# Performance work log

Hardware: AMD Instinct MI355X
Metric: run time of the kernel (lower is better)

## Reference

```python
import jax, jax.numpy as jnp
import numpy as np

N_NODES = 50000
N_EDGES = 800000
IN_FEAT = 128
HEADS = 4
UNITS = 16
LEAKY_ALPHA = 0.2  # tf.nn.leaky_relu default


def setup_inputs() -> dict:
    key = jax.random.key(0)
    k1, k2, k3, k4, k5 = jax.random.split(key, 5)
    x = jax.random.normal(k1, (N_NODES, IN_FEAT), dtype=jnp.float32)
    edge_index = jax.random.randint(k2, (N_EDGES, 2), 0, N_NODES, dtype=jnp.int32)
    # Dense kernel (glorot-ish scaling), no bias (use_bias=False)
    W = jax.random.normal(k3, (IN_FEAT, HEADS * UNITS), dtype=jnp.float32) * (1.0 / np.sqrt(IN_FEAT))
    glorot = np.sqrt(2.0 / (1 + UNITS)).astype(np.float32)
    att_w1 = jax.random.normal(k4, (HEADS, 1, UNITS), dtype=jnp.float32) * glorot
    att_w2 = jax.random.normal(k5, (HEADS, 1, UNITS), dtype=jnp.float32) * glorot
    return {"x": x, "edge_index": edge_index, "W": W, "att_w1": att_w1, "att_w2": att_w2}


def reference(x, edge_index, W, att_w1, att_w2):
    n_nodes = x.shape[0]
    h = x @ W  # [N, H*U]
    snd_idx = edge_index[:, 0]
    rcv_idx = edge_index[:, 1]
    # gather per-edge features, split into heads -> [H, E, U]
    sender = h[snd_idx].reshape(-1, HEADS, UNITS).transpose(1, 0, 2)
    receiver = h[rcv_idx].reshape(-1, HEADS, UNITS).transpose(1, 0, 2)
    # per-edge, per-head attention logits [H, E]
    att = jnp.sum(att_w1 * sender, axis=-1) + jnp.sum(att_w2 * receiver, axis=-1)
    att = jnp.where(att > 0, att, LEAKY_ALPHA * att)
    # segment softmax over receiver neighborhoods, per head
    seg_max = jax.vmap(lambda a: jax.ops.segment_max(a, rcv_idx, num_segments=n_nodes))(att)  # [H, N]
    e = jnp.exp(att - seg_max[:, rcv_idx])
    denom = jax.vmap(lambda a: jax.ops.segment_sum(a, rcv_idx, num_segments=n_nodes))(e)  # [H, N]
    alpha = e / denom[:, rcv_idx]  # [H, E]
    # weighted scatter-sum of sender features -> [H, N, U]
    out = jax.vmap(lambda v: jax.ops.segment_sum(v, rcv_idx, num_segments=n_nodes))(sender * alpha[:, :, None])
    # concat heads -> [N, H*U]; activation is None (identity)
    return out.transpose(1, 0, 2).reshape(n_nodes, HEADS * UNITS)
```

## Files before the change

kernel.cpp:

```cpp
#include <hip/hip_runtime.h>
#include <math.h>

#define N_NODES 50000
#define N_EDGES 800000
#define IN_FEAT 128
#define HEADS   4
#define UNITS   16
#define OUTF    64
#define LEAKY   0.2f

#define CAP     64
#define GEMM_BLKS 782
#define A_BLOCKS  391
#define EPB     8

typedef __attribute__((ext_vector_type(8))) short bf16x8;
typedef __attribute__((ext_vector_type(4))) float f32x4;

__device__ __forceinline__ unsigned short f2bf(float f) {
    unsigned u = __float_as_uint(f);
    unsigned r = u + 0x7FFFu + ((u >> 16) & 1u);
    return (unsigned short)(r >> 16);
}

__global__ __launch_bounds__(256) void prep(const float* __restrict__ W,
                                            unsigned short* __restrict__ Wt_g,
                                            int* __restrict__ node_cnt) {
    int idx = blockIdx.x * 256 + threadIdx.x;
    if (idx < N_NODES) node_cnt[idx] = 0;
    if (idx < IN_FEAT * OUTF) {
        int k = idx >> 6, c = idx & 63;
        Wt_g[c * IN_FEAT + k] = f2bf(W[idx]);
    }
}

__global__ __launch_bounds__(256) void fused_gemm_scatter(const float* __restrict__ x,
                                                          const unsigned short* __restrict__ Wt_g,
                                                          const float* __restrict__ w1,
                                                          const float* __restrict__ w2,
                                                          const int2* __restrict__ ei,
                                                          unsigned short* __restrict__ hg,
                                                          float* __restrict__ a1,
                                                          float* __restrict__ a2,
                                                          int* __restrict__ node_cnt,
                                                          int* __restrict__ csr) {
    const int t = threadIdx.x;

    if (blockIdx.x >= GEMM_BLKS) {
        const int e0 = (blockIdx.x - GEMM_BLKS) * 2048;
        #pragma unroll
        for (int j = 0; j < EPB; ++j) {
            int e = e0 + t + j * 256;
            if (e < N_EDGES) {
                int2 ed = ei[e];
                int p = atomicAdd(&node_cnt[ed.y], 1);
                if (p < CAP) csr[(size_t)ed.y * CAP + p] = ed.x;
            }
        }
        return;
    }

    __shared__ unsigned short xl[64 * 136];
    __shared__ unsigned short wt[64 * 136];

    const int node0 = blockIdx.x * 64;

    #pragma unroll
    for (int it = 0; it < 8; ++it) {
        int idx = t + 256 * it;
        int r = idx >> 5, q = idx & 31;
        int node = node0 + r;
        float4 v = make_float4(0.f, 0.f, 0.f, 0.f);
        if (node < N_NODES) v = *(const float4*)(x + (size_t)node * IN_FEAT + q * 4);
        ushort4 b;
        b.x = f2bf(v.x); b.y = f2bf(v.y); b.z = f2bf(v.z); b.w = f2bf(v.w);
        *(ushort4*)&xl[r * 136 + q * 4] = b;
    }
    {
        const ushort4* Wt4 = (const ushort4*)Wt_g;
        #pragma unroll
        for (int it = 0; it < 8; ++it) {
            int idx = t + 256 * it;
            int c = idx >> 5, u = idx & 31;
            *(ushort4*)&wt[c * 136 + u * 4] = Wt4[idx];
        }
    }
    __syncthreads();

    const int lane = t & 63, wv = t >> 6;
    const int m = lane & 15, quad = lane >> 4;
    const int n0 = wv * 16;

    f32x4 acc[4] = {{0,0,0,0},{0,0,0,0},{0,0,0,0},{0,0,0,0}};
    #pragma unroll
    for (int kc = 0; kc < 4; ++kc) {
        bf16x8 af = *(bf16x8*)&xl[(n0 + m) * 136 + kc * 32 + quad * 8];
        #pragma unroll
        for (int ct = 0; ct < 4; ++ct) {
            bf16x8 bfr = *(bf16x8*)&wt[(ct * 16 + m) * 136 + kc * 32 + quad * 8];
            acc[ct] = __builtin_amdgcn_mfma_f32_16x16x32_bf16(af, bfr, acc[ct], 0, 0, 0);
        }
    }

    #pragma unroll
    for (int ct = 0; ct < 4; ++ct) {
        const float u1 = w1[ct * 16 + m];
        const float u2 = w2[ct * 16 + m];
        #pragma unroll
        for (int r = 0; r < 4; ++r) {
            float p1 = acc[ct][r] * u1;
            float p2 = acc[ct][r] * u2;
            p1 += __shfl_xor(p1, 1, 64); p1 += __shfl_xor(p1, 2, 64);
            p1 += __shfl_xor(p1, 4, 64); p1 += __shfl_xor(p1, 8, 64);
            p2 += __shfl_xor(p2, 1, 64); p2 += __shfl_xor(p2, 2, 64);
            p2 += __shfl_xor(p2, 4, 64); p2 += __shfl_xor(p2, 8, 64);
            if (m == 0) {
                int node = node0 + n0 + quad * 4 + r;
                if (node < N_NODES) {
                    a1[node * 4 + ct] = p1;
                    a2[node * 4 + ct] = p2;
                }
            }
        }
    }

    __syncthreads();
    unsigned short* hl = xl;
    #pragma unroll
    for (int ct = 0; ct < 4; ++ct)
        #pragma unroll
        for (int r = 0; r < 4; ++r)
            hl[(n0 + quad * 4 + r) * 72 + ct * 16 + m] = f2bf(acc[ct][r]);
    __syncthreads();
    #pragma unroll
    for (int it = 0; it < 2; ++it) {
        int u = t + 256 * it;
        int r = u >> 3, cg = u & 7;
        int node = node0 + r;
        if (node < N_NODES)
            *(uint4*)&hg[(size_t)node * OUTF + cg * 8] = *(uint4*)&hl[r * 72 + cg * 8];
    }
}

__global__ __launch_bounds__(256, 8) void gather_kernel(const int* __restrict__ node_cnt,
                                                        const int* __restrict__ csr,
                                                        const float* __restrict__ a1,
                                                        const float* __restrict__ a2,
                                                        const unsigned short* __restrict__ h,
                                                        float* __restrict__ out) {
    const int wave = threadIdx.x >> 6;
    const int lane = threadIdx.x & 63;
    const int n = blockIdx.x * 4 + wave;
    if (n >= N_NODES) return;
    const int sub  = lane >> 3;
    const int li   = lane & 7;
    const int head = li >> 1;
    const int cn   = min(node_cnt[n], CAP);
    if (cn <= 0) {
        if (sub == 0) {
            *(float4*)(out + (size_t)n * OUTF + li * 8)     = make_float4(0.f, 0.f, 0.f, 0.f);
            *(float4*)(out + (size_t)n * OUTF + li * 8 + 4) = make_float4(0.f, 0.f, 0.f, 0.f);
        }
        return;
    }
    const int base = n * CAP;
    const float a2h = a2[n * 4 + head];
    const uint4* h4 = (const uint4*)h;

    float acc[8] = {0.f,0.f,0.f,0.f,0.f,0.f,0.f,0.f};
    float den = 0.f;

    for (int i0 = 0; i0 < cn; i0 += 16) {
        #pragma unroll
        for (int g = 0; g < 2; ++g) {
            int er = i0 + g * 8 + sub;
            int ec = min(er, cn - 1);
            int s = csr[base + ec];
            float t0 = a1[s * 4 + head] + a2h;
            t0 = t0 > 0.f ? t0 : LEAKY * t0;
            float e = (er < cn) ? __expf(t0) : 0.f;
            uint4 hv = h4[(unsigned)(s * 8 + li)];
            const unsigned hw[4] = {hv.x, hv.y, hv.z, hv.w};
            #pragma unroll
            for (int q = 0; q < 4; ++q) {
                acc[q*2+0] = fmaf(e, __uint_as_float(hw[q] << 16),         acc[q*2+0]);
                acc[q*2+1] = fmaf(e, __uint_as_float(hw[q] & 0xFFFF0000u), acc[q*2+1]);
            }
            den += e;
        }
    }

    #pragma unroll
    for (int off = 8; off <= 32; off <<= 1) {
        #pragma unroll
        for (int q = 0; q < 8; ++q) acc[q] += __shfl_xor(acc[q], off, 64);
        den += __shfl_xor(den, off, 64);
    }

    if (sub == 0) {
        float inv = 1.f / den;
        *(float4*)(out + (size_t)n * OUTF + li * 8) =
            make_float4(acc[0] * inv, acc[1] * inv, acc[2] * inv, acc[3] * inv);
        *(float4*)(out + (size_t)n * OUTF + li * 8 + 4) =
            make_float4(acc[4] * inv, acc[5] * inv, acc[6] * inv, acc[7] * inv);
    }
}

extern "C" void kernel_launch(void* const* d_in, const int* in_sizes, int n_in,
                              void* d_out, int out_size, void* d_ws, size_t ws_size,
                              hipStream_t stream) {
    const float* x  = (const float*)d_in[0];
    const int2*  ei = (const int2*)d_in[1];
    const float* W  = (const float*)d_in[2];
    const float* w1 = (const float*)d_in[3];
    const float* w2 = (const float*)d_in[4];
    float* out = (float*)d_out;

    unsigned short* h    = (unsigned short*)d_ws;
    float* a1            = (float*)(h + (size_t)N_NODES * OUTF);
    float* a2            = a1 + (size_t)N_NODES * HEADS;
    unsigned short* Wt_g = (unsigned short*)(a2 + (size_t)N_NODES * HEADS);
    int* node_cnt        = (int*)(Wt_g + IN_FEAT * OUTF);
    int* csr             = node_cnt + N_NODES;

    prep<<<196, 256, 0, stream>>>(W, Wt_g, node_cnt);
    fused_gemm_scatter<<<GEMM_BLKS + A_BLOCKS, 256, 0, stream>>>(x, Wt_g, w1, w2, ei,
                                                                 h, a1, a2,
                                                                 node_cnt, csr);
    gather_kernel<<<(N_NODES + 3) / 4, 256, 0, stream>>>(node_cnt, csr, a1, a2, h, out);
}
```

Baseline: 153.4 us.

## Replace per-node CSR with 128-node edge buckets and shared-memory atomic aggregation

Edge binning now groups edges into 391 buckets of 128 receiver nodes. Each block builds a local histogram and prefix scan, reserves space with one global atomic per bucket, and writes staged edges out contiguously, instead of doing one global atomic per edge into a capped per-node CSR. The aggregate kernel processes one bucket per 1024-thread block and accumulates weighted features and denominators with LDS float atomics into a swizzled tile, then normalizes and writes out. This removes the 64-neighbor cap and the per-edge global atomics. In exchange it adds heavy LDS atomic contention, only 391 blocks of parallelism, and a fixed bucket capacity of 2560 that random inputs should stay under (average about 2046).

```diff
diff --git a/kernel.cpp b/kernel.cpp
--- a/kernel.cpp
+++ b/kernel.cpp
@@ -9,7 +9,11 @@
 #define OUTF    64
 #define LEAKY   0.2f
 
-#define CAP     64
+#define BSH     7
+#define BNODES  128
+#define NB      391
+#define NBP     512
+#define BCAP    2560
 #define GEMM_BLKS 782
 #define A_BLOCKS  391
 #define EPB     8
@@ -23,18 +27,23 @@
     return (unsigned short)(r >> 16);
 }
 
+union SharedU {
+    struct { unsigned short xl[64 * 136]; unsigned short wt[64 * 136]; } g;
+    struct { int2 stage[2048]; int hist[NBP], cur[NBP], adj[NBP], s[256]; } a;
+};
+
 __global__ __launch_bounds__(256) void prep(const float* __restrict__ W,
                                             unsigned short* __restrict__ Wt_g,
-                                            int* __restrict__ node_cnt) {
+                                            int* __restrict__ bucket_cnt) {
     int idx = blockIdx.x * 256 + threadIdx.x;
-    if (idx < N_NODES) node_cnt[idx] = 0;
+    if (idx < NBP) bucket_cnt[idx] = 0;
     if (idx < IN_FEAT * OUTF) {
         int k = idx >> 6, c = idx & 63;
         Wt_g[c * IN_FEAT + k] = f2bf(W[idx]);
     }
 }
 
-__global__ __launch_bounds__(256) void fused_gemm_scatter(const float* __restrict__ x,
+__global__ __launch_bounds__(256) void fused_gemm_bucketA(const float* __restrict__ x,
                                                           const unsigned short* __restrict__ Wt_g,
                                                           const float* __restrict__ w1,
                                                           const float* __restrict__ w2,
@@ -42,28 +51,70 @@
                                                           unsigned short* __restrict__ hg,
                                                           float* __restrict__ a1,
                                                           float* __restrict__ a2,
-                                                          int* __restrict__ node_cnt,
-                                                          int* __restrict__ csr) {
+                                                          int* __restrict__ bucket_cnt,
+                                                          int2* __restrict__ buckets) {
+    __shared__ SharedU sh;
     const int t = threadIdx.x;
 
     if (blockIdx.x >= GEMM_BLKS) {
         const int e0 = (blockIdx.x - GEMM_BLKS) * 2048;
+        sh.a.hist[t] = 0; sh.a.hist[t + 256] = 0;
+        __syncthreads();
+
+        int2 ed[EPB]; int bk[EPB];
         #pragma unroll
         for (int j = 0; j < EPB; ++j) {
             int e = e0 + t + j * 256;
             if (e < N_EDGES) {
-                int2 ed = ei[e];
-                int p = atomicAdd(&node_cnt[ed.y], 1);
-                if (p < CAP) csr[(size_t)ed.y * CAP + p] = ed.x;
+                ed[j] = ei[e];
+                bk[j] = ed[j].y >> BSH;
+                atomicAdd(&sh.a.hist[bk[j]], 1);
+            } else bk[j] = -1;
+        }
+        __syncthreads();
+        const int h0 = sh.a.hist[2 * t], h1 = sh.a.hist[2 * t + 1];
+        const int lsum = h0 + h1;
+        sh.a.s[t] = lsum;
+        __syncthreads();
+        #pragma unroll
+        for (int off = 1; off < 256; off <<= 1) {
+            int u = (t >= off) ? sh.a.s[t - off] : 0;
+            __syncthreads();
+            sh.a.s[t] += u;
+            __syncthreads();
+        }
+        const int base = sh.a.s[t] - lsum;
+        const int ex0 = base, ex1 = base + h0;
+        sh.a.cur[2 * t] = ex0; sh.a.cur[2 * t + 1] = ex1;
+        if (2 * t < NB) {
+            int g0 = atomicAdd(&bucket_cnt[2 * t], h0);
+            sh.a.adj[2 * t] = g0 - ex0;
+        }
+        if (2 * t + 1 < NB) {
+            int g1 = atomicAdd(&bucket_cnt[2 * t + 1], h1);
+            sh.a.adj[2 * t + 1] = g1 - ex1;
+        }
+        __syncthreads();
+        #pragma unroll
+        for (int j = 0; j < EPB; ++j) {
+            if (bk[j] >= 0) {
+                int p = atomicAdd(&sh.a.cur[bk[j]], 1);
+                sh.a.stage[p] = ed[j];
             }
         }
+        __syncthreads();
+        const int total = min(2048, N_EDGES - e0);
+        for (int i = t; i < total; i += 256) {
+            int2 vv = sh.a.stage[i];
+            int b = vv.y >> BSH;
+            buckets[(size_t)(b * BCAP + sh.a.adj[b] + i)] = vv;
+        }
         return;
     }
 
-    __shared__ unsigned short xl[64 * 136];
-    __shared__ unsigned short wt[64 * 136];
-
     const int node0 = blockIdx.x * 64;
+    unsigned short* xl = sh.g.xl;
+    unsigned short* wt = sh.g.wt;
 
     #pragma unroll
     for (int it = 0; it < 8; ++it) {
@@ -125,7 +176,7 @@
     }
 
     __syncthreads();
-    unsigned short* hl = xl;
+    unsigned short* hl = sh.g.xl;
     #pragma unroll
     for (int ct = 0; ct < 4; ++ct)
         #pragma unroll
@@ -142,67 +193,62 @@
     }
 }
 
-__global__ __launch_bounds__(256, 8) void gather_kernel(const int* __restrict__ node_cnt,
-                                                        const int* __restrict__ csr,
-                                                        const float* __restrict__ a1,
-                                                        const float* __restrict__ a2,
-                                                        const unsigned short* __restrict__ h,
-                                                        float* __restrict__ out) {
-    const int wave = threadIdx.x >> 6;
-    const int lane = threadIdx.x & 63;
-    const int n = blockIdx.x * 4 + wave;
-    if (n >= N_NODES) return;
-    const int sub  = lane >> 3;
-    const int li   = lane & 7;
+__global__ __launch_bounds__(1024) void aggregate(const int2* __restrict__ buckets,
+                                                  const int* __restrict__ bucket_cnt,
+                                                  const float* __restrict__ a1,
+                                                  const float* __restrict__ a2,
+                                                  const unsigned short* __restrict__ h,
+                                                  float* __restrict__ out) {
+    __shared__ float acc[BNODES * OUTF];
+    __shared__ float den[BNODES * HEADS];
+    const int b = blockIdx.x;
+    const int t = threadIdx.x;
+    const int cnt = bucket_cnt[b];
+
+    #pragma unroll
+    for (int u = t; u < BNODES * OUTF; u += 1024) acc[u] = 0.f;
+    if (t < BNODES * HEADS) den[t] = 0.f;
+    __syncthreads();
+
+    const int slot = t >> 3;
+    const int li   = t & 7;
     const int head = li >> 1;
-    const int cn   = min(node_cnt[n], CAP);
-    if (cn <= 0) {
-        if (sub == 0) {
-            *(float4*)(out + (size_t)n * OUTF + li * 8)     = make_float4(0.f, 0.f, 0.f, 0.f);
-            *(float4*)(out + (size_t)n * OUTF + li * 8 + 4) = make_float4(0.f, 0.f, 0.f, 0.f);
-        }
-        return;
-    }
-    const int base = n * CAP;
-    const float a2h = a2[n * 4 + head];
     const uint4* h4 = (const uint4*)h;
 
-    float acc[8] = {0.f,0.f,0.f,0.f,0.f,0.f,0.f,0.f};
-    float den = 0.f;
-
-    for (int i0 = 0; i0 < cn; i0 += 16) {
-        #pragma unroll
-        for (int g = 0; g < 2; ++g) {
-            int er = i0 + g * 8 + sub;
-            int ec = min(er, cn - 1);
-            int s = csr[base + ec];
-            float t0 = a1[s * 4 + head] + a2h;
-            t0 = t0 > 0.f ? t0 : LEAKY * t0;
-            float e = (er < cn) ? __expf(t0) : 0.f;
-            uint4 hv = h4[(unsigned)(s * 8 + li)];
-            const unsigned hw[4] = {hv.x, hv.y, hv.z, hv.w};
-            #pragma unroll
-            for (int q = 0; q < 4; ++q) {
-                acc[q*2+0] = fmaf(e, __uint_as_float(hw[q] << 16),         acc[q*2+0]);
-                acc[q*2+1] = fmaf(e, __uint_as_float(hw[q] & 0xFFFF0000u), acc[q*2+1]);
-            }
-            den += e;
-        }
-    }
-
-    #pragma unroll
-    for (int off = 8; off <= 32; off <<= 1) {
-        #pragma unroll
-        for (int q = 0; q < 8; ++q) acc[q] += __shfl_xor(acc[q], off, 64);
-        den += __shfl_xor(den, off, 64);
-    }
-
-    if (sub == 0) {
-        float inv = 1.f / den;
-        *(float4*)(out + (size_t)n * OUTF + li * 8) =
-            make_float4(acc[0] * inv, acc[1] * inv, acc[2] * inv, acc[3] * inv);
-        *(float4*)(out + (size_t)n * OUTF + li * 8 + 4) =
-            make_float4(acc[4] * inv, acc[5] * inv, acc[6] * inv, acc[7] * inv);
+    for (int i = slot; i < cnt; i += 128) {
+        int2 ed = buckets[(size_t)b * BCAP + i];
+        const int s   = ed.x;
+        const int loc = ed.y & (BNODES - 1);
+        float t0 = a1[s * 4 + head] + a2[ed.y * 4 + head];
+        t0 = t0 > 0.f ? t0 : LEAKY * t0;
+        const float e = __expf(t0);
+        uint4 hv = h4[(unsigned)s * 8 + li];
+        const unsigned hw[4] = {hv.x, hv.y, hv.z, hv.w};
+        float* arow = &acc[loc * OUTF];
+        const int sw = loc & 63;
+        #pragma unroll
+        for (int q = 0; q < 4; ++q) {
+            int c0 = li * 8 + 2 * q;
+            atomicAdd(&arow[(c0)     ^ sw], e * __uint_as_float(hw[q] << 16));
+            atomicAdd(&arow[(c0 + 1) ^ sw], e * __uint_as_float(hw[q] & 0xFFFF0000u));
+        }
+        if (!(li & 1)) atomicAdd(&den[loc * 4 + head], e);
+    }
+    __syncthreads();
+
+    if (t < BNODES * HEADS) {
+        float d = den[t];
+        den[t] = (d > 0.f) ? 1.f / d : 0.f;
+    }
+    __syncthreads();
+
+    #pragma unroll
+    for (int u = t; u < BNODES * OUTF; u += 1024) {
+        int loc = u >> 6, col = u & 63;
+        int node = b * BNODES + loc;
+        if (node < N_NODES)
+            out[(size_t)node * OUTF + col] =
+                acc[loc * OUTF + (col ^ (loc & 63))] * den[loc * 4 + (col >> 4)];
     }
 }
 
@@ -220,12 +266,12 @@
     float* a1            = (float*)(h + (size_t)N_NODES * OUTF);
     float* a2            = a1 + (size_t)N_NODES * HEADS;
     unsigned short* Wt_g = (unsigned short*)(a2 + (size_t)N_NODES * HEADS);
-    int* node_cnt        = (int*)(Wt_g + IN_FEAT * OUTF);
-    int* csr             = node_cnt + N_NODES;
-
-    prep<<<196, 256, 0, stream>>>(W, Wt_g, node_cnt);
-    fused_gemm_scatter<<<GEMM_BLKS + A_BLOCKS, 256, 0, stream>>>(x, Wt_g, w1, w2, ei,
+    int*   bucket_cnt    = (int*)(Wt_g + IN_FEAT * OUTF);
+    int2*  buckets       = (int2*)(bucket_cnt + NBP);
+
+    prep<<<32, 256, 0, stream>>>(W, Wt_g, bucket_cnt);
+    fused_gemm_bucketA<<<GEMM_BLKS + A_BLOCKS, 256, 0, stream>>>(x, Wt_g, w1, w2, ei,
                                                                  h, a1, a2,
-                                                                 node_cnt, csr);
-    gather_kernel<<<(N_NODES + 3) / 4, 256, 0, stream>>>(node_cnt, csr, a1, a2, h, out);
-}
+                                                                 bucket_cnt, buckets);
+    aggregate<<<NB, 1024, 0, stream>>>(buckets, bucket_cnt, a1, a2, h, out);
+}
```

New measurement: 468.1 us. 205% more time.
